# Optimization experiments

Measured on AMD Instinct MI355X. Metric: run time of the kernel, lower is better.

## Reference

```python
import jax, jax.numpy as jnp
import numpy as np

NEG = -1000.0  # fill value for unmatched (type_mask != ti) entries

B, N, R = 4, 48, 16
T = 2 * R + 1          # 33 transition channels
Nc, L = 80, 3          # chains, chain length
Nt, Ni = 16, 5         # triples, chains per triple (uniform c_sections)


def setup_inputs() -> dict:
    key = jax.random.key(0)
    k1, k2, k3, k4, k5 = jax.random.split(key, 5)
    transitions = jax.random.normal(k1, (B, N, N, T), dtype=jnp.float32)
    type_mask = jax.random.randint(k2, (B, N, N, R), 0, 2, dtype=jnp.int32)
    rules = jax.random.randint(k3, (Nc, L), 0, T, dtype=jnp.int32)
    # stacked per-triple weights [Nt, Ni] (orig: ParameterList of [Ni,1]) and biases [Nt]
    weights = jax.random.normal(k4, (Nt, Ni), dtype=jnp.float32) / np.sqrt(Ni)
    biases = jax.random.uniform(k5, (Nt,), dtype=jnp.float32, minval=-1.0, maxval=1.0)
    return {"transitions": transitions, "type_mask": type_mask, "rules": rules,
            "weights": weights, "biases": biases}


def path_scores(transitions, rules):
    """Tropical (max-plus) chain DP.
    transitions: [B,N,N,T], rules: [Nc,L] -> scores [B,N,N,Nc]
    scores[b,x,y,c] = max over intermediate nodes of sum of hop scores.
    """
    Lc = rules.shape[1]
    hops = [transitions[..., rules[:, l]] for l in range(Lc)]  # each [B,N,N,Nc]
    # max-plus "matmul": s[b,x,y,c] = max_k hops0[b,x,k,c] + hops1[b,k,y,c]
    s = jnp.max(hops[0][:, :, :, None, :] + hops[1][:, None, :, :, :], axis=2)
    for l in range(2, Lc):
        s = jnp.max(s[:, :, :, None, :] + hops[l][:, None, :, :, :], axis=2)
    return s


def reference(transitions, type_mask, rules, weights, biases):
    # scores over all chains, exponentiated: [B,N,N,Nc]
    s = jnp.exp(path_scores(transitions, rules))
    # group chains by triple (uniform sections): [B,N,N,Nt,Ni]
    s = s.reshape(s.shape[0], s.shape[1], s.shape[2], Nt, Ni)
    # per-triple weighted sum + bias; one triple per relation so Nt == R
    comb = jnp.einsum('bxytc,tc->bxyt', s, weights) + biases  # [B,N,N,R]
    # masked_scatter: write score where type_mask[...,i] == ti (== 0 here), else -1000
    out = jnp.where(type_mask == 0, comb, NEG)
    return out
```

## Files before the change

kernel.cpp:

```cpp
#include <hip/hip_runtime.h>
#include <cmath>

#define BB 4
#define NN 48
#define PP (NN * NN)
#define NP 49
#define TT 33
#define RR 16
#define NC 80
#define NI 5
#define NEG (-1000.0f)

__global__ __launch_bounds__(256) void transpose_kernel(
    const float* __restrict__ trans,
    float*       __restrict__ tpose)
{
    __shared__ float tile[64 * TT];
    const int blk = blockIdx.x;
    const int b   = blk / 36;
    const int p0  = (blk - b * 36) * 64;

    const float4* src = (const float4*)(trans + ((size_t)b * PP + p0) * TT);
    for (int j = threadIdx.x; j < 64 * TT / 4; j += 256)
        ((float4*)tile)[j] = src[j];
    __syncthreads();

    for (int j = threadIdx.x; j < TT * 64; j += 256) {
        const int t  = j >> 6;
        const int pl = j & 63;
        tpose[((size_t)b * TT + t) * PP + p0 + pl] = tile[pl * TT + t];
    }
}

__global__ __launch_bounds__(192) void chain_dp_kernel(
    const float* __restrict__ tpose,
    const int*   __restrict__ rules,
    const float* __restrict__ weights,
    float*       __restrict__ sw)
{
    __shared__ float H0T[NN * NP];
    __shared__ float H1 [PP];
    __shared__ float H2 [PP];
    __shared__ float S1T[NN * NP];

    const int bc = blockIdx.x;
    const int b  = bc / NC;
    const int c  = bc - b * NC;

    const int r0 = rules[c * 3 + 0];
    const int r1 = rules[c * 3 + 1];
    const int r2 = rules[c * 3 + 2];

    const float* p0 = tpose + ((size_t)b * TT + r0) * PP;
    const float* p1 = tpose + ((size_t)b * TT + r1) * PP;
    const float* p2 = tpose + ((size_t)b * TT + r2) * PP;

    for (int j = threadIdx.x; j < PP / 4; j += 192) {
        ((float4*)H1)[j] = ((const float4*)p1)[j];
        ((float4*)H2)[j] = ((const float4*)p2)[j];
        const float4 v0 = ((const float4*)p0)[j];
        const int x = (4 * j) / NN;
        const int k = (4 * j) - x * NN;
        H0T[(k + 0) * NP + x] = v0.x;
        H0T[(k + 1) * NP + x] = v0.y;
        H0T[(k + 2) * NP + x] = v0.z;
        H0T[(k + 3) * NP + x] = v0.w;
    }
    __syncthreads();

    const int tx = threadIdx.x & 15;
    const int ty = threadIdx.x >> 4;
    const int x0 = tx * 3;
    const int y0 = ty * 4;

    float acc[3][4];
    #pragma unroll
    for (int jx = 0; jx < 3; ++jx)
        #pragma unroll
        for (int jy = 0; jy < 4; ++jy) acc[jx][jy] = -INFINITY;

    #pragma unroll 4
    for (int kp = 0; kp < NN / 2; ++kp) {
        const int k = kp * 2;
        float a0[3], a1[3];
        #pragma unroll
        for (int jx = 0; jx < 3; ++jx) {
            a0[jx] = H0T[k * NP + x0 + jx];
            a1[jx] = H0T[(k + 1) * NP + x0 + jx];
        }
        const float4 bv0 = *(const float4*)&H1[k * NN + y0];
        const float4 bv1 = *(const float4*)&H1[(k + 1) * NN + y0];
        const float b0[4] = {bv0.x, bv0.y, bv0.z, bv0.w};
        const float b1[4] = {bv1.x, bv1.y, bv1.z, bv1.w};
        #pragma unroll
        for (int jx = 0; jx < 3; ++jx)
            #pragma unroll
            for (int jy = 0; jy < 4; ++jy)
                acc[jx][jy] = fmaxf(acc[jx][jy],
                                    fmaxf(a0[jx] + b0[jy], a1[jx] + b1[jy]));
    }

    #pragma unroll
    for (int jx = 0; jx < 3; ++jx)
        #pragma unroll
        for (int jy = 0; jy < 4; ++jy)
            S1T[(y0 + jy) * NP + x0 + jx] = acc[jx][jy];
    __syncthreads();

    float acc2[3][4];
    #pragma unroll
    for (int jx = 0; jx < 3; ++jx)
        #pragma unroll
        for (int jy = 0; jy < 4; ++jy) acc2[jx][jy] = -INFINITY;

    #pragma unroll 4
    for (int kp = 0; kp < NN / 2; ++kp) {
        const int k = kp * 2;
        float a0[3], a1[3];
        #pragma unroll
        for (int jx = 0; jx < 3; ++jx) {
            a0[jx] = S1T[k * NP + x0 + jx];
            a1[jx] = S1T[(k + 1) * NP + x0 + jx];
        }
        const float4 bv0 = *(const float4*)&H2[k * NN + y0];
        const float4 bv1 = *(const float4*)&H2[(k + 1) * NN + y0];
        const float b0[4] = {bv0.x, bv0.y, bv0.z, bv0.w};
        const float b1[4] = {bv1.x, bv1.y, bv1.z, bv1.w};
        #pragma unroll
        for (int jx = 0; jx < 3; ++jx)
            #pragma unroll
            for (int jy = 0; jy < 4; ++jy)
                acc2[jx][jy] = fmaxf(acc2[jx][jy],
                                     fmaxf(a0[jx] + b0[jy], a1[jx] + b1[jy]));
    }

    const float wgt = weights[c];
    float* outp = sw + (size_t)bc * PP;
    #pragma unroll
    for (int jx = 0; jx < 3; ++jx) {
        float4 o;
        o.x = __expf(acc2[jx][0]) * wgt;
        o.y = __expf(acc2[jx][1]) * wgt;
        o.z = __expf(acc2[jx][2]) * wgt;
        o.w = __expf(acc2[jx][3]) * wgt;
        *(float4*)&outp[(x0 + jx) * NN + y0] = o;
    }
}

__global__ __launch_bounds__(256) void combine_kernel(
    const float* __restrict__ sw,
    const int*   __restrict__ mask,
    const float* __restrict__ biases,
    float*       __restrict__ out)
{
    const int tq = threadIdx.x >> 7;
    const int pl = blockIdx.x * 128 + (threadIdx.x & 127);
    if (pl >= BB * PP) return;
    const int b = pl / PP;
    const int p = pl - b * PP;

    const float* base = sw + (size_t)b * NC * PP + p;

    float acc[8];
    #pragma unroll
    for (int tt = 0; tt < 8; ++tt) {
        const int t = tq * 8 + tt;
        float s = biases[t];
        #pragma unroll
        for (int i = 0; i < NI; ++i)
            s += base[(size_t)(t * NI + i) * PP];
        acc[tt] = s;
    }

    const int4* m4 = (const int4*)(mask + (size_t)pl * RR + tq * 8);
    float4*     o4 = (float4*)(out + (size_t)pl * RR + tq * 8);
    #pragma unroll
    for (int q = 0; q < 2; ++q) {
        const int4 m = m4[q];
        float4 o;
        o.x = (m.x == 0) ? acc[q * 4 + 0] : NEG;
        o.y = (m.y == 0) ? acc[q * 4 + 1] : NEG;
        o.z = (m.z == 0) ? acc[q * 4 + 2] : NEG;
        o.w = (m.w == 0) ? acc[q * 4 + 3] : NEG;
        o4[q] = o;
    }
}

extern "C" void kernel_launch(void* const* d_in, const int* in_sizes, int n_in,
                              void* d_out, int out_size, void* d_ws, size_t ws_size,
                              hipStream_t stream)
{
    const float* trans   = (const float*)d_in[0];
    const int*   mask    = (const int*)  d_in[1];
    const int*   rules   = (const int*)  d_in[2];
    const float* weights = (const float*)d_in[3];
    const float* biases  = (const float*)d_in[4];
    float* out = (float*)d_out;

    float* tpose = (float*)d_ws;
    float* sw    = tpose + (size_t)BB * TT * PP;

    transpose_kernel<<<BB * 36, 256, 0, stream>>>(trans, tpose);

    chain_dp_kernel<<<BB * NC, 192, 0, stream>>>(tpose, rules, weights, sw);

    const int total2 = BB * PP * 2;
    combine_kernel<<<(total2 + 255) / 256, 256, 0, stream>>>(sw, mask, biases, out);
}
```

Measured before the change: 75.23 us.

## Split chain DP blocks over x-halves and widen combine kernel grid

The chain DP kernel now launches two blocks per (batch, chain), each computing half of the x rows with a 3x2 per-thread tile instead of 3x4. This doubles the block count to improve occupancy and fill more CUs on a GPU with many compute units. The cost is that each block still loads the full H1 and H2 matrices, duplicating those loads, and the second DP stage recomputes only its half. The combine kernel now gives each thread 4 triples instead of 8, doubling the number of blocks.

```diff
diff --git a/kernel.cpp b/kernel.cpp
--- a/kernel.cpp
+++ b/kernel.cpp
@@ -4,13 +4,15 @@
 #define BB 4
 #define NN 48
 #define PP (NN * NN)
-#define NP 49
 #define TT 33
 #define RR 16
 #define NC 80
 #define NI 5
 #define NEG (-1000.0f)
 
+#define XS 24
+#define XP 25
+
 __global__ __launch_bounds__(256) void transpose_kernel(
     const float* __restrict__ trans,
     float*       __restrict__ tpose)
@@ -38,46 +40,51 @@
     const float* __restrict__ weights,
     float*       __restrict__ sw)
 {
-    __shared__ float H0T[NN * NP];
+    __shared__ float H0T[NN * XP];
     __shared__ float H1 [PP];
     __shared__ float H2 [PP];
-    __shared__ float S1T[NN * NP];
-
-    const int bc = blockIdx.x;
-    const int b  = bc / NC;
-    const int c  = bc - b * NC;
+    __shared__ float S1T[NN * XP];
+
+    const int blk = blockIdx.x;
+    const int bc  = blk >> 1;
+    const int xh  = blk & 1;
+    const int b   = bc / NC;
+    const int c   = bc - b * NC;
+    const int xbase = xh * XS;
 
     const int r0 = rules[c * 3 + 0];
     const int r1 = rules[c * 3 + 1];
     const int r2 = rules[c * 3 + 2];
 
-    const float* p0 = tpose + ((size_t)b * TT + r0) * PP;
+    const float* p0 = tpose + ((size_t)b * TT + r0) * PP + xbase * NN;
     const float* p1 = tpose + ((size_t)b * TT + r1) * PP;
     const float* p2 = tpose + ((size_t)b * TT + r2) * PP;
 
     for (int j = threadIdx.x; j < PP / 4; j += 192) {
         ((float4*)H1)[j] = ((const float4*)p1)[j];
         ((float4*)H2)[j] = ((const float4*)p2)[j];
+    }
+    for (int j = threadIdx.x; j < XS * NN / 4; j += 192) {
         const float4 v0 = ((const float4*)p0)[j];
-        const int x = (4 * j) / NN;
-        const int k = (4 * j) - x * NN;
-        H0T[(k + 0) * NP + x] = v0.x;
-        H0T[(k + 1) * NP + x] = v0.y;
-        H0T[(k + 2) * NP + x] = v0.z;
-        H0T[(k + 3) * NP + x] = v0.w;
+        const int xl = (4 * j) / NN;
+        const int k  = (4 * j) - xl * NN;
+        H0T[(k + 0) * XP + xl] = v0.x;
+        H0T[(k + 1) * XP + xl] = v0.y;
+        H0T[(k + 2) * XP + xl] = v0.z;
+        H0T[(k + 3) * XP + xl] = v0.w;
     }
     __syncthreads();
 
-    const int tx = threadIdx.x & 15;
-    const int ty = threadIdx.x >> 4;
+    const int tx = threadIdx.x & 7;
+    const int ty = threadIdx.x >> 3;
     const int x0 = tx * 3;
-    const int y0 = ty * 4;
-
-    float acc[3][4];
-    #pragma unroll
-    for (int jx = 0; jx < 3; ++jx)
-        #pragma unroll
-        for (int jy = 0; jy < 4; ++jy) acc[jx][jy] = -INFINITY;
+    const int y0 = ty * 2;
+
+    float acc[3][2];
+    #pragma unroll
+    for (int jx = 0; jx < 3; ++jx) {
+        acc[jx][0] = -INFINITY; acc[jx][1] = -INFINITY;
+    }
 
     #pragma unroll 4
     for (int kp = 0; kp < NN / 2; ++kp) {
@@ -85,33 +92,30 @@
         float a0[3], a1[3];
         #pragma unroll
         for (int jx = 0; jx < 3; ++jx) {
-            a0[jx] = H0T[k * NP + x0 + jx];
-            a1[jx] = H0T[(k + 1) * NP + x0 + jx];
-        }
-        const float4 bv0 = *(const float4*)&H1[k * NN + y0];
-        const float4 bv1 = *(const float4*)&H1[(k + 1) * NN + y0];
-        const float b0[4] = {bv0.x, bv0.y, bv0.z, bv0.w};
-        const float b1[4] = {bv1.x, bv1.y, bv1.z, bv1.w};
-        #pragma unroll
-        for (int jx = 0; jx < 3; ++jx)
-            #pragma unroll
-            for (int jy = 0; jy < 4; ++jy)
-                acc[jx][jy] = fmaxf(acc[jx][jy],
-                                    fmaxf(a0[jx] + b0[jy], a1[jx] + b1[jy]));
-    }
-
-    #pragma unroll
-    for (int jx = 0; jx < 3; ++jx)
-        #pragma unroll
-        for (int jy = 0; jy < 4; ++jy)
-            S1T[(y0 + jy) * NP + x0 + jx] = acc[jx][jy];
+            a0[jx] = H0T[k * XP + x0 + jx];
+            a1[jx] = H0T[(k + 1) * XP + x0 + jx];
+        }
+        const float2 bv0 = *(const float2*)&H1[k * NN + y0];
+        const float2 bv1 = *(const float2*)&H1[(k + 1) * NN + y0];
+        #pragma unroll
+        for (int jx = 0; jx < 3; ++jx) {
+            acc[jx][0] = fmaxf(acc[jx][0], fmaxf(a0[jx] + bv0.x, a1[jx] + bv1.x));
+            acc[jx][1] = fmaxf(acc[jx][1], fmaxf(a0[jx] + bv0.y, a1[jx] + bv1.y));
+        }
+    }
+
+    #pragma unroll
+    for (int jx = 0; jx < 3; ++jx) {
+        S1T[(y0 + 0) * XP + x0 + jx] = acc[jx][0];
+        S1T[(y0 + 1) * XP + x0 + jx] = acc[jx][1];
+    }
     __syncthreads();
 
-    float acc2[3][4];
-    #pragma unroll
-    for (int jx = 0; jx < 3; ++jx)
-        #pragma unroll
-        for (int jy = 0; jy < 4; ++jy) acc2[jx][jy] = -INFINITY;
+    float acc2[3][2];
+    #pragma unroll
+    for (int jx = 0; jx < 3; ++jx) {
+        acc2[jx][0] = -INFINITY; acc2[jx][1] = -INFINITY;
+    }
 
     #pragma unroll 4
     for (int kp = 0; kp < NN / 2; ++kp) {
@@ -119,31 +123,26 @@
         float a0[3], a1[3];
         #pragma unroll
         for (int jx = 0; jx < 3; ++jx) {
-            a0[jx] = S1T[k * NP + x0 + jx];
-            a1[jx] = S1T[(k + 1) * NP + x0 + jx];
-        }
-        const float4 bv0 = *(const float4*)&H2[k * NN + y0];
-        const float4 bv1 = *(const float4*)&H2[(k + 1) * NN + y0];
-        const float b0[4] = {bv0.x, bv0.y, bv0.z, bv0.w};
-        const float b1[4] = {bv1.x, bv1.y, bv1.z, bv1.w};
-        #pragma unroll
-        for (int jx = 0; jx < 3; ++jx)
-            #pragma unroll
-            for (int jy = 0; jy < 4; ++jy)
-                acc2[jx][jy] = fmaxf(acc2[jx][jy],
-                                     fmaxf(a0[jx] + b0[jy], a1[jx] + b1[jy]));
+            a0[jx] = S1T[k * XP + x0 + jx];
+            a1[jx] = S1T[(k + 1) * XP + x0 + jx];
+        }
+        const float2 bv0 = *(const float2*)&H2[k * NN + y0];
+        const float2 bv1 = *(const float2*)&H2[(k + 1) * NN + y0];
+        #pragma unroll
+        for (int jx = 0; jx < 3; ++jx) {
+            acc2[jx][0] = fmaxf(acc2[jx][0], fmaxf(a0[jx] + bv0.x, a1[jx] + bv1.x));
+            acc2[jx][1] = fmaxf(acc2[jx][1], fmaxf(a0[jx] + bv0.y, a1[jx] + bv1.y));
+        }
     }
 
     const float wgt = weights[c];
     float* outp = sw + (size_t)bc * PP;
     #pragma unroll
     for (int jx = 0; jx < 3; ++jx) {
-        float4 o;
+        float2 o;
         o.x = __expf(acc2[jx][0]) * wgt;
         o.y = __expf(acc2[jx][1]) * wgt;
-        o.z = __expf(acc2[jx][2]) * wgt;
-        o.w = __expf(acc2[jx][3]) * wgt;
-        *(float4*)&outp[(x0 + jx) * NN + y0] = o;
+        *(float2*)&outp[(xbase + x0 + jx) * NN + y0] = o;
     }
 }
 
@@ -153,18 +152,17 @@
     const float* __restrict__ biases,
     float*       __restrict__ out)
 {
-    const int tq = threadIdx.x >> 7;
-    const int pl = blockIdx.x * 128 + (threadIdx.x & 127);
-    if (pl >= BB * PP) return;
+    const int quad = threadIdx.x >> 6;
+    const int pl   = blockIdx.x * 64 + (threadIdx.x & 63);
     const int b = pl / PP;
     const int p = pl - b * PP;
 
     const float* base = sw + (size_t)b * NC * PP + p;
 
-    float acc[8];
-    #pragma unroll
-    for (int tt = 0; tt < 8; ++tt) {
-        const int t = tq * 8 + tt;
+    float acc[4];
+    #pragma unroll
+    for (int tt = 0; tt < 4; ++tt) {
+        const int t = quad * 4 + tt;
         float s = biases[t];
         #pragma unroll
         for (int i = 0; i < NI; ++i)
@@ -172,18 +170,13 @@
         acc[tt] = s;
     }
 
-    const int4* m4 = (const int4*)(mask + (size_t)pl * RR + tq * 8);
-    float4*     o4 = (float4*)(out + (size_t)pl * RR + tq * 8);
-    #pragma unroll
-    for (int q = 0; q < 2; ++q) {
-        const int4 m = m4[q];
-        float4 o;
-        o.x = (m.x == 0) ? acc[q * 4 + 0] : NEG;
-        o.y = (m.y == 0) ? acc[q * 4 + 1] : NEG;
-        o.z = (m.z == 0) ? acc[q * 4 + 2] : NEG;
-        o.w = (m.w == 0) ? acc[q * 4 + 3] : NEG;
-        o4[q] = o;
-    }
+    const int4 m = *(const int4*)(mask + (size_t)pl * RR + quad * 4);
+    float4 o;
+    o.x = (m.x == 0) ? acc[0] : NEG;
+    o.y = (m.y == 0) ? acc[1] : NEG;
+    o.z = (m.z == 0) ? acc[2] : NEG;
+    o.w = (m.w == 0) ? acc[3] : NEG;
+    *(float4*)(out + (size_t)pl * RR + quad * 4) = o;
 }
 
 extern "C" void kernel_launch(void* const* d_in, const int* in_sizes, int n_in,
@@ -202,8 +195,7 @@
 
     transpose_kernel<<<BB * 36, 256, 0, stream>>>(trans, tpose);
 
-    chain_dp_kernel<<<BB * NC, 192, 0, stream>>>(tpose, rules, weights, sw);
-
-    const int total2 = BB * PP * 2;
-    combine_kernel<<<(total2 + 255) / 256, 256, 0, stream>>>(sw, mask, biases, out);
-}
+    chain_dp_kernel<<<BB * NC * 2, 192, 0, stream>>>(tpose, rules, weights, sw);
+
+    combine_kernel<<<BB * PP / 64, 256, 0, stream>>>(sw, mask, biases, out);
+}
```

Result: no change. 75.38 us (+0.2%).

## Fuse transpose, chain DP and combine into one cooperative kernel

Applied to the files above, without the earlier changes.

Replaces the three kernel launches with a single cooperative kernel. The transpose pass is removed: each block gathers its three rule channels directly from the strided [B,N,N,T] input into shared memory. A grid-wide sync then separates the DP phase from the combine phase, which is remapped to four relations per thread. This removes two launch overheads and the intermediate transposed buffer, at the cost of strided scalar gathers (stride 33 floats), a grid barrier, and a requirement that all 320 blocks be co-resident.

```diff
diff --git a/kernel.cpp b/kernel.cpp
--- a/kernel.cpp
+++ b/kernel.cpp
@@ -1,5 +1,8 @@
 #include <hip/hip_runtime.h>
+#include <hip/hip_cooperative_groups.h>
 #include <cmath>
+
+namespace cg = cooperative_groups;
 
 #define BB 4
 #define NN 48
@@ -11,178 +14,156 @@
 #define NI 5
 #define NEG (-1000.0f)
 
-__global__ __launch_bounds__(256) void transpose_kernel(
+#define NBLK 320
+#define NTH  192
+
+__global__ __launch_bounds__(NTH) void fused_kernel(
     const float* __restrict__ trans,
-    float*       __restrict__ tpose)
-{
-    __shared__ float tile[64 * TT];
-    const int blk = blockIdx.x;
-    const int b   = blk / 36;
-    const int p0  = (blk - b * 36) * 64;
-
-    const float4* src = (const float4*)(trans + ((size_t)b * PP + p0) * TT);
-    for (int j = threadIdx.x; j < 64 * TT / 4; j += 256)
-        ((float4*)tile)[j] = src[j];
-    __syncthreads();
-
-    for (int j = threadIdx.x; j < TT * 64; j += 256) {
-        const int t  = j >> 6;
-        const int pl = j & 63;
-        tpose[((size_t)b * TT + t) * PP + p0 + pl] = tile[pl * TT + t];
-    }
-}
-
-__global__ __launch_bounds__(192) void chain_dp_kernel(
-    const float* __restrict__ tpose,
     const int*   __restrict__ rules,
     const float* __restrict__ weights,
+    const float* __restrict__ biases,
+    const int*   __restrict__ mask,
+    float*       __restrict__ out,
     float*       __restrict__ sw)
 {
+    cg::grid_group grid = cg::this_grid();
+
     __shared__ float H0T[NN * NP];
     __shared__ float H1 [PP];
     __shared__ float H2 [PP];
     __shared__ float S1T[NN * NP];
 
-    const int bc = blockIdx.x;
-    const int b  = bc / NC;
-    const int c  = bc - b * NC;
+    {
+        const int bc = blockIdx.x;
+        const int b  = bc / NC;
+        const int c  = bc - b * NC;
 
-    const int r0 = rules[c * 3 + 0];
-    const int r1 = rules[c * 3 + 1];
-    const int r2 = rules[c * 3 + 2];
+        const int r0 = rules[c * 3 + 0];
+        const int r1 = rules[c * 3 + 1];
+        const int r2 = rules[c * 3 + 2];
 
-    const float* p0 = tpose + ((size_t)b * TT + r0) * PP;
-    const float* p1 = tpose + ((size_t)b * TT + r1) * PP;
-    const float* p2 = tpose + ((size_t)b * TT + r2) * PP;
+        const float* tb = trans + (size_t)b * PP * TT;
 
-    for (int j = threadIdx.x; j < PP / 4; j += 192) {
-        ((float4*)H1)[j] = ((const float4*)p1)[j];
-        ((float4*)H2)[j] = ((const float4*)p2)[j];
-        const float4 v0 = ((const float4*)p0)[j];
-        const int x = (4 * j) / NN;
-        const int k = (4 * j) - x * NN;
-        H0T[(k + 0) * NP + x] = v0.x;
-        H0T[(k + 1) * NP + x] = v0.y;
-        H0T[(k + 2) * NP + x] = v0.z;
-        H0T[(k + 3) * NP + x] = v0.w;
-    }
-    __syncthreads();
+        for (int i = threadIdx.x; i < PP; i += NTH) {
+            const int x = i / NN;
+            const int k = i - x * NN;
+            const size_t base = (size_t)i * TT;
+            H0T[k * NP + x] = tb[base + r0];
+            H1[i]           = tb[base + r1];
+            H2[i]           = tb[base + r2];
+        }
+        __syncthreads();
 
-    const int tx = threadIdx.x & 15;
-    const int ty = threadIdx.x >> 4;
-    const int x0 = tx * 3;
-    const int y0 = ty * 4;
+        const int tx = threadIdx.x & 15;
+        const int ty = threadIdx.x >> 4;
+        const int x0 = tx * 3;
+        const int y0 = ty * 4;
 
-    float acc[3][4];
-    #pragma unroll
-    for (int jx = 0; jx < 3; ++jx)
+        float acc[3][4];
         #pragma unroll
-        for (int jy = 0; jy < 4; ++jy) acc[jx][jy] = -INFINITY;
+        for (int jx = 0; jx < 3; ++jx)
+            #pragma unroll
+            for (int jy = 0; jy < 4; ++jy) acc[jx][jy] = -INFINITY;
 
-    #pragma unroll 4
-    for (int kp = 0; kp < NN / 2; ++kp) {
-        const int k = kp * 2;
-        float a0[3], a1[3];
-        #pragma unroll
-        for (int jx = 0; jx < 3; ++jx) {
-            a0[jx] = H0T[k * NP + x0 + jx];
-            a1[jx] = H0T[(k + 1) * NP + x0 + jx];
+        #pragma unroll 4
+        for (int kp = 0; kp < NN / 2; ++kp) {
+            const int k = kp * 2;
+            float a0[3], a1[3];
+            #pragma unroll
+            for (int jx = 0; jx < 3; ++jx) {
+                a0[jx] = H0T[k * NP + x0 + jx];
+                a1[jx] = H0T[(k + 1) * NP + x0 + jx];
+            }
+            const float4 bv0 = *(const float4*)&H1[k * NN + y0];
+            const float4 bv1 = *(const float4*)&H1[(k + 1) * NN + y0];
+            const float b0[4] = {bv0.x, bv0.y, bv0.z, bv0.w};
+            const float b1[4] = {bv1.x, bv1.y, bv1.z, bv1.w};
+            #pragma unroll
+            for (int jx = 0; jx < 3; ++jx)
+                #pragma unroll
+                for (int jy = 0; jy < 4; ++jy)
+                    acc[jx][jy] = fmaxf(acc[jx][jy],
+                                        fmaxf(a0[jx] + b0[jy], a1[jx] + b1[jy]));
         }
-        const float4 bv0 = *(const float4*)&H1[k * NN + y0];
-        const float4 bv1 = *(const float4*)&H1[(k + 1) * NN + y0];
-        const float b0[4] = {bv0.x, bv0.y, bv0.z, bv0.w};
-        const float b1[4] = {bv1.x, bv1.y, bv1.z, bv1.w};
+
         #pragma unroll
         for (int jx = 0; jx < 3; ++jx)
             #pragma unroll
             for (int jy = 0; jy < 4; ++jy)
-                acc[jx][jy] = fmaxf(acc[jx][jy],
-                                    fmaxf(a0[jx] + b0[jy], a1[jx] + b1[jy]));
-    }
+                S1T[(y0 + jy) * NP + x0 + jx] = acc[jx][jy];
+        __syncthreads();
 
-    #pragma unroll
-    for (int jx = 0; jx < 3; ++jx)
-        #pragma unroll
-        for (int jy = 0; jy < 4; ++jy)
-            S1T[(y0 + jy) * NP + x0 + jx] = acc[jx][jy];
-    __syncthreads();
-
-    float acc2[3][4];
-    #pragma unroll
-    for (int jx = 0; jx < 3; ++jx)
-        #pragma unroll
-        for (int jy = 0; jy < 4; ++jy) acc2[jx][jy] = -INFINITY;
-
-    #pragma unroll 4
-    for (int kp = 0; kp < NN / 2; ++kp) {
-        const int k = kp * 2;
-        float a0[3], a1[3];
-        #pragma unroll
-        for (int jx = 0; jx < 3; ++jx) {
-            a0[jx] = S1T[k * NP + x0 + jx];
-            a1[jx] = S1T[(k + 1) * NP + x0 + jx];
-        }
-        const float4 bv0 = *(const float4*)&H2[k * NN + y0];
-        const float4 bv1 = *(const float4*)&H2[(k + 1) * NN + y0];
-        const float b0[4] = {bv0.x, bv0.y, bv0.z, bv0.w};
-        const float b1[4] = {bv1.x, bv1.y, bv1.z, bv1.w};
+        float acc2[3][4];
         #pragma unroll
         for (int jx = 0; jx < 3; ++jx)
             #pragma unroll
-            for (int jy = 0; jy < 4; ++jy)
-                acc2[jx][jy] = fmaxf(acc2[jx][jy],
-                                     fmaxf(a0[jx] + b0[jy], a1[jx] + b1[jy]));
+            for (int jy = 0; jy < 4; ++jy) acc2[jx][jy] = -INFINITY;
+
+        #pragma unroll 4
+        for (int kp = 0; kp < NN / 2; ++kp) {
+            const int k = kp * 2;
+            float a0[3], a1[3];
+            #pragma unroll
+            for (int jx = 0; jx < 3; ++jx) {
+                a0[jx] = S1T[k * NP + x0 + jx];
+                a1[jx] = S1T[(k + 1) * NP + x0 + jx];
+            }
+            const float4 bv0 = *(const float4*)&H2[k * NN + y0];
+            const float4 bv1 = *(const float4*)&H2[(k + 1) * NN + y0];
+            const float b0[4] = {bv0.x, bv0.y, bv0.z, bv0.w};
+            const float b1[4] = {bv1.x, bv1.y, bv1.z, bv1.w};
+            #pragma unroll
+            for (int jx = 0; jx < 3; ++jx)
+                #pragma unroll
+                for (int jy = 0; jy < 4; ++jy)
+                    acc2[jx][jy] = fmaxf(acc2[jx][jy],
+                                         fmaxf(a0[jx] + b0[jy], a1[jx] + b1[jy]));
+        }
+
+        const float wgt = weights[c];
+        float* outp = sw + (size_t)bc * PP;
+        #pragma unroll
+        for (int jx = 0; jx < 3; ++jx) {
+            float4 o;
+            o.x = __expf(acc2[jx][0]) * wgt;
+            o.y = __expf(acc2[jx][1]) * wgt;
+            o.z = __expf(acc2[jx][2]) * wgt;
+            o.w = __expf(acc2[jx][3]) * wgt;
+            *(float4*)&outp[(x0 + jx) * NN + y0] = o;
+        }
     }
 
-    const float wgt = weights[c];
-    float* outp = sw + (size_t)bc * PP;
-    #pragma unroll
-    for (int jx = 0; jx < 3; ++jx) {
-        float4 o;
-        o.x = __expf(acc2[jx][0]) * wgt;
-        o.y = __expf(acc2[jx][1]) * wgt;
-        o.z = __expf(acc2[jx][2]) * wgt;
-        o.w = __expf(acc2[jx][3]) * wgt;
-        *(float4*)&outp[(x0 + jx) * NN + y0] = o;
-    }
-}
+    grid.sync();
 
-__global__ __launch_bounds__(256) void combine_kernel(
-    const float* __restrict__ sw,
-    const int*   __restrict__ mask,
-    const float* __restrict__ biases,
-    float*       __restrict__ out)
-{
-    const int tq = threadIdx.x >> 7;
-    const int pl = blockIdx.x * 128 + (threadIdx.x & 127);
-    if (pl >= BB * PP) return;
-    const int b = pl / PP;
-    const int p = pl - b * PP;
+    {
+        const int tid = blockIdx.x * NTH + threadIdx.x;
+        if (tid < BB * PP * 4) {
+            const int quad = (tid >> 6) & 3;
+            const int pl   = (tid >> 8) * 64 + (tid & 63);
+            const int b = pl / PP;
+            const int p = pl - b * PP;
 
-    const float* base = sw + (size_t)b * NC * PP + p;
+            const float* base = sw + (size_t)b * NC * PP + p;
 
-    float acc[8];
-    #pragma unroll
-    for (int tt = 0; tt < 8; ++tt) {
-        const int t = tq * 8 + tt;
-        float s = biases[t];
-        #pragma unroll
-        for (int i = 0; i < NI; ++i)
-            s += base[(size_t)(t * NI + i) * PP];
-        acc[tt] = s;
-    }
+            float acc[4];
+            #pragma unroll
+            for (int tt = 0; tt < 4; ++tt) {
+                const int t = quad * 4 + tt;
+                float s = biases[t];
+                #pragma unroll
+                for (int i = 0; i < NI; ++i)
+                    s += base[(size_t)(t * NI + i) * PP];
+                acc[tt] = s;
+            }
 
-    const int4* m4 = (const int4*)(mask + (size_t)pl * RR + tq * 8);
-    float4*     o4 = (float4*)(out + (size_t)pl * RR + tq * 8);
-    #pragma unroll
-    for (int q = 0; q < 2; ++q) {
-        const int4 m = m4[q];
-        float4 o;
-        o.x = (m.x == 0) ? acc[q * 4 + 0] : NEG;
-        o.y = (m.y == 0) ? acc[q * 4 + 1] : NEG;
-        o.z = (m.z == 0) ? acc[q * 4 + 2] : NEG;
-        o.w = (m.w == 0) ? acc[q * 4 + 3] : NEG;
-        o4[q] = o;
+            const int4 m = *(const int4*)(mask + (size_t)pl * RR + quad * 4);
+            float4 o;
+            o.x = (m.x == 0) ? acc[0] : NEG;
+            o.y = (m.y == 0) ? acc[1] : NEG;
+            o.z = (m.z == 0) ? acc[2] : NEG;
+            o.w = (m.w == 0) ? acc[3] : NEG;
+            *(float4*)(out + (size_t)pl * RR + quad * 4) = o;
+        }
     }
 }
 
@@ -196,14 +177,10 @@
     const float* weights = (const float*)d_in[3];
     const float* biases  = (const float*)d_in[4];
     float* out = (float*)d_out;
+    float* sw  = (float*)d_ws;
 
-    float* tpose = (float*)d_ws;
-    float* sw    = tpose + (size_t)BB * TT * PP;
-
-    transpose_kernel<<<BB * 36, 256, 0, stream>>>(trans, tpose);
-
-    chain_dp_kernel<<<BB * NC, 192, 0, stream>>>(tpose, rules, weights, sw);
-
-    const int total2 = BB * PP * 2;
-    combine_kernel<<<(total2 + 255) / 256, 256, 0, stream>>>(sw, mask, biases, out);
+    void* args[] = { (void*)&trans, (void*)&rules, (void*)&weights,
+                     (void*)&biases, (void*)&mask, (void*)&out, (void*)&sw };
+    hipLaunchCooperativeKernel((const void*)fused_kernel,
+                               dim3(NBLK), dim3(NTH), args, 0, stream);
 }
```

New measurement: 126.5 us. 1.68x slower.
